# Performance work log

Hardware: AMD Instinct MI355X
Metric: run time of the kernel (lower is better)

## Reference

```python
import jax, jax.numpy as jnp
import numpy as np


def setup_inputs() -> dict:
    key = jax.random.key(0)
    k1, k2, k3, k4, k5, k6 = jax.random.split(key, 6)
    b, L, h, eh, M, N = 16, 256, 256, 64, 128, 128
    X = jax.random.normal(k1, (b, L, h), dtype=jnp.float32)
    E = jax.random.normal(k2, (b, L, L, eh), dtype=jnp.float32)
    A = jax.random.uniform(k3, (b, L, L), dtype=jnp.float32)
    w = jax.random.normal(k4, (b, L, 1), dtype=jnp.float32)
    mask = jnp.ones((b, L, L), dtype=bool)
    mol_lens = jax.random.randint(k5, (b, 2), 64, M + 1, dtype=jnp.int32)
    # force one row to the max so M,N match torch.max(mol_lens) exactly
    mol_lens = mol_lens.at[0].set(jnp.array([M, N], dtype=jnp.int32))
    return {"X": X, "E": E, "A": A, "w": w, "mask": mask,
            "mol_lens": mol_lens, "M": M, "N": N}


def reference(X, E, A, w, mask, mol_lens, M, N):
    b, L, h = X.shape
    eh = E.shape[-1]
    l0 = mol_lens[:, 0][:, None]            # [b,1]
    l1 = mol_lens[:, 1][:, None]
    p1 = jnp.arange(2 * M)[None, :]         # [1,2M]
    p2 = jnp.arange(2 * N)[None, :]         # [1,2N]

    # duplicate-and-pad source indices (note: X2 copies X[:, :l1], per source)
    src1 = jnp.clip(jnp.where(p1 < l0, p1, p1 - l0), 0, L - 1)          # [b,2M]
    srcX2 = jnp.clip(jnp.where(p2 < l1, p2, p2 - l1), 0, L - 1)         # [b,2N]
    srcE2 = jnp.clip(l0 + jnp.where(p2 < l1, p2, p2 - l1), 0, L - 1)    # [b,2N]
    valid1 = p1 < 2 * l0                    # [b,2M]
    valid2 = p2 < 2 * l1                    # [b,2N]

    bi = jnp.arange(b)[:, None]
    X1 = jnp.where(valid1[..., None], X[bi, src1], 0.0)                 # [b,2M,h]
    X2 = jnp.where(valid2[..., None], X[bi, srcX2], 0.0)                # [b,2N,h]

    # block-diagonal validity: (first copy x first copy) | (second x second)
    f1 = p1 < l0
    s1 = (p1 >= l0) & valid1
    blk1 = (f1[:, :, None] & f1[:, None, :]) | (s1[:, :, None] & s1[:, None, :])
    f2 = p2 < l1
    s2 = (p2 >= l1) & valid2
    blk2 = (f2[:, :, None] & f2[:, None, :]) | (s2[:, :, None] & s2[:, None, :])

    bii = jnp.arange(b)[:, None, None]
    g1 = E[bii, src1[:, :, None], src1[:, None, :]]                     # [b,2M,2M,eh]
    E1 = jnp.where(blk1[..., None], g1, 0.0)
    A1 = jnp.where(blk1, A[bii, src1[:, :, None], src1[:, None, :]], 0.0)
    g2 = E[bii, srcE2[:, :, None], srcE2[:, None, :]]                   # [b,2N,2N,eh]
    E2 = jnp.where(blk2[..., None], g2, 0.0)
    A2 = jnp.where(blk2, A[bii, srcE2[:, :, None], srcE2[:, None, :]], 0.0)

    w1 = jnp.zeros((b, 2 * M, 1), X.dtype)
    w2 = jnp.zeros((b, 2 * N, 1), X.dtype)

    # cross-copy masks on padded tensors
    mask1 = ~((f1[:, :, None] & s1[:, None, :]) | (s1[:, :, None] & f1[:, None, :]))
    mask2 = ~((f2[:, :, None] & s2[:, None, :]) | (s2[:, :, None] & f2[:, None, :]))

    # in-place edits of input mask: True on [:l0,:l0] and [l0:,l0:], False on cross
    q = jnp.arange(L)[None, :]
    lsum = l0 + l1
    left = q < l0                           # [b,L]
    midd = (q >= l0) & (q < lsum)
    cond_true = (left[:, :, None] & left[:, None, :]) | ((~left)[:, :, None] & (~left)[:, None, :])
    cond_false = (left[:, :, None] & midd[:, None, :]) | (midd[:, :, None] & left[:, None, :])
    mask_out = jnp.where(cond_true, True, jnp.where(cond_false, False, mask))

    return (X1, X2, E1, E2, A1, A2, mask1, mask2, w1, w2, mask_out)
```

## Files before the change

kernel.cpp:

```cpp
#include <hip/hip_runtime.h>


#define OFF_X1   0
#define OFF_X2   1048576
#define OFF_E1   2097152
#define OFF_E2   69206016
#define OFF_A1   136314880
#define OFF_A2   137363456
#define OFF_M1   138412032
#define OFF_M2   139460608
#define OFF_W1   140509184
#define OFF_MO   140517376

#define OFF_E1_V4 (OFF_E1 / 4)
#define OFF_E2_V4 (OFF_E2 / 4)

typedef float f32x4 __attribute__((ext_vector_type(4)));

__global__ __launch_bounds__(256) void fused_kernel(
    const f32x4* __restrict__ E,
    const float* __restrict__ X,
    const float* __restrict__ A,
    const int*   __restrict__ mask,
    const int*   __restrict__ mol_lens,
    float*       __restrict__ out)
{
    const int bb  = blockIdx.x;
    const int tid = threadIdx.x;

    const int i = bb >> 12;
    const int p = (bb >> 4) & 255;
    const int q = ((bb & 15) << 4) | (tid >> 4);
    const int c = tid & 15;
    const int t = bb * 256 + tid;

    const int l0 = mol_lens[i * 2];
    const int l1 = mol_lens[i * 2 + 1];

    f32x4* outv4 = (f32x4*)out;

    {
        const bool fp = p < l0, sp = !fp && (p < 2 * l0);
        const bool fq = q < l0, sq = !fq && (q < 2 * l0);
        f32x4 v = (f32x4)(0.f, 0.f, 0.f, 0.f);
        if ((fp && fq) || (sp && sq)) {
            const int ip = fp ? p : p - l0;
            const int iq = fq ? q : q - l0;
            v = E[((i * 256 + ip) * 256 + iq) * 16 + c];
        }
        __builtin_nontemporal_store(v, &outv4[OFF_E1_V4 + t]);
    }

    {
        const bool fp = p < l1, sp = !fp && (p < 2 * l1);
        const bool fq = q < l1, sq = !fq && (q < 2 * l1);
        f32x4 v = (f32x4)(0.f, 0.f, 0.f, 0.f);
        if ((fp && fq) || (sp && sq)) {
            int ip = l0 + (fp ? p : p - l1); if (ip > 255) ip = 255;
            int iq = l0 + (fq ? q : q - l1); if (iq > 255) iq = 255;
            v = E[((i * 256 + ip) * 256 + iq) * 16 + c];
        }
        __builtin_nontemporal_store(v, &outv4[OFF_E2_V4 + t]);
    }

    if (bb < 4096) {
        const int ts = t;
        const int qs = tid;
        const int ps = bb & 255;
        const int is = bb >> 8;

        const int sl0 = mol_lens[is * 2];
        const int sl1 = mol_lens[is * 2 + 1];

        const bool v1  = ps < 2 * sl0;
        const int  s1p = (ps < sl0) ? ps : ps - sl0;
        __builtin_nontemporal_store(
            v1 ? X[(is * 256 + s1p) * 256 + qs] : 0.f, &out[OFF_X1 + ts]);

        const bool v2  = ps < 2 * sl1;
        const int  s2p = (ps < sl1) ? ps : ps - sl1;
        __builtin_nontemporal_store(
            v2 ? X[(is * 256 + s2p) * 256 + qs] : 0.f, &out[OFF_X2 + ts]);

        const bool f1p = ps < sl0, s1pb = (!f1p) && v1;
        const bool f1q = qs < sl0, s1qb = (!f1q) && (qs < 2 * sl0);
        const int  s1q = f1q ? qs : qs - sl0;
        const bool blk1 = (f1p && f1q) || (s1pb && s1qb);
        __builtin_nontemporal_store(
            blk1 ? A[(is * 256 + s1p) * 256 + s1q] : 0.f, &out[OFF_A1 + ts]);
        __builtin_nontemporal_store(
            ((f1p && s1qb) || (s1pb && f1q)) ? 0.f : 1.f, &out[OFF_M1 + ts]);

        const bool f2p = ps < sl1, s2pb = (!f2p) && v2;
        const bool f2q = qs < sl1, s2qb = (!f2q) && (qs < 2 * sl1);
        int e2p = sl0 + (f2p ? ps : ps - sl1); if (e2p > 255) e2p = 255;
        int e2q = sl0 + (f2q ? qs : qs - sl1); if (e2q > 255) e2q = 255;
        const bool blk2 = (f2p && f2q) || (s2pb && s2qb);
        __builtin_nontemporal_store(
            blk2 ? A[(is * 256 + e2p) * 256 + e2q] : 0.f, &out[OFF_A2 + ts]);
        __builtin_nontemporal_store(
            ((f2p && s2qb) || (s2pb && f2q)) ? 0.f : 1.f, &out[OFF_M2 + ts]);

        const bool leftp = ps < sl0, leftq = qs < sl0;
        const int  lsum  = sl0 + sl1;
        const bool middp = (!leftp) && (ps < lsum);
        const bool middq = (!leftq) && (qs < lsum);
        const bool ct = (leftp && leftq) || ((!leftp) && (!leftq));
        const bool cf = (leftp && middq) || (middp && leftq);
        float mv;
        if (ct)      mv = 1.f;
        else if (cf) mv = 0.f;
        else         mv = (mask[ts] != 0) ? 1.f : 0.f;
        __builtin_nontemporal_store(mv, &out[OFF_MO + ts]);

        if (ts < 8192)
            __builtin_nontemporal_store(0.f, &out[OFF_W1 + ts]);
    }
}

extern "C" void kernel_launch(void* const* d_in, const int* in_sizes, int n_in,
                              void* d_out, int out_size, void* d_ws, size_t ws_size,
                              hipStream_t stream) {
    const float* X        = (const float*)d_in[0];
    const float* E        = (const float*)d_in[1];
    const float* A        = (const float*)d_in[2];
    const int*   mask     = (const int*)d_in[4];
    const int*   mol_lens = (const int*)d_in[5];

    float* out = (float*)d_out;

    fused_kernel<<<65536, 256, 0, stream>>>(
        (const f32x4*)E, X, A, mask, mol_lens, out);
}
```

Baseline: 694.5 us.

## Split E gather into separate kernel reading each source once, writing two copies

```diff
diff --git a/kernel.cpp b/kernel.cpp
--- a/kernel.cpp
+++ b/kernel.cpp
@@ -17,8 +17,7 @@
 
 typedef float f32x4 __attribute__((ext_vector_type(4)));
 
-__global__ __launch_bounds__(256) void fused_kernel(
-    const f32x4* __restrict__ E,
+__global__ __launch_bounds__(256) void fill_small_kernel(
     const float* __restrict__ X,
     const float* __restrict__ A,
     const int*   __restrict__ mask,
@@ -31,36 +30,25 @@
     const int i = bb >> 12;
     const int p = (bb >> 4) & 255;
     const int q = ((bb & 15) << 4) | (tid >> 4);
-    const int c = tid & 15;
     const int t = bb * 256 + tid;
 
     const int l0 = mol_lens[i * 2];
     const int l1 = mol_lens[i * 2 + 1];
 
     f32x4* outv4 = (f32x4*)out;
+    const f32x4 zero = (f32x4)(0.f, 0.f, 0.f, 0.f);
 
     {
         const bool fp = p < l0, sp = !fp && (p < 2 * l0);
         const bool fq = q < l0, sq = !fq && (q < 2 * l0);
-        f32x4 v = (f32x4)(0.f, 0.f, 0.f, 0.f);
-        if ((fp && fq) || (sp && sq)) {
-            const int ip = fp ? p : p - l0;
-            const int iq = fq ? q : q - l0;
-            v = E[((i * 256 + ip) * 256 + iq) * 16 + c];
-        }
-        __builtin_nontemporal_store(v, &outv4[OFF_E1_V4 + t]);
+        if (!((fp && fq) || (sp && sq)))
+            __builtin_nontemporal_store(zero, &outv4[OFF_E1_V4 + t]);
     }
-
     {
         const bool fp = p < l1, sp = !fp && (p < 2 * l1);
         const bool fq = q < l1, sq = !fq && (q < 2 * l1);
-        f32x4 v = (f32x4)(0.f, 0.f, 0.f, 0.f);
-        if ((fp && fq) || (sp && sq)) {
-            int ip = l0 + (fp ? p : p - l1); if (ip > 255) ip = 255;
-            int iq = l0 + (fq ? q : q - l1); if (iq > 255) iq = 255;
-            v = E[((i * 256 + ip) * 256 + iq) * 16 + c];
-        }
-        __builtin_nontemporal_store(v, &outv4[OFF_E2_V4 + t]);
+        if (!((fp && fq) || (sp && sq)))
+            __builtin_nontemporal_store(zero, &outv4[OFF_E2_V4 + t]);
     }
 
     if (bb < 4096) {
@@ -118,6 +106,47 @@
     }
 }
 
+__global__ __launch_bounds__(256) void gather_kernel(
+    const f32x4* __restrict__ E,
+    const int*   __restrict__ mol_lens,
+    float*       __restrict__ out)
+{
+    const int bb  = blockIdx.x;
+    const int tid = threadIdx.x;
+
+    const int c     = tid & 15;
+    const int iqo   = tid >> 4;
+    const int chunk = bb & 7;
+    const int ip    = (bb >> 3) & 127;
+    const int i     = bb >> 10;
+    const int iq    = chunk * 16 + iqo;
+
+    const int l0 = mol_lens[i * 2];
+    const int l1 = mol_lens[i * 2 + 1];
+
+    f32x4* outv4 = (f32x4*)out;
+
+    if (ip < l0) {
+        if (iq < l0) {
+            const f32x4 v = E[((i * 256 + ip) * 256 + iq) * 16 + c];
+            const int d1 = OFF_E1_V4 + ((i * 256 + ip) * 256 + iq) * 16 + c;
+            __builtin_nontemporal_store(v, &outv4[d1]);
+            const int d2 = OFF_E1_V4 + ((i * 256 + ip + l0) * 256 + (iq + l0)) * 16 + c;
+            __builtin_nontemporal_store(v, &outv4[d2]);
+        }
+    }
+
+    if (ip < l1) {
+        if (iq < l1) {
+            const f32x4 v = E[((i * 256 + l0 + ip) * 256 + (l0 + iq)) * 16 + c];
+            const int d1 = OFF_E2_V4 + ((i * 256 + ip) * 256 + iq) * 16 + c;
+            __builtin_nontemporal_store(v, &outv4[d1]);
+            const int d2 = OFF_E2_V4 + ((i * 256 + ip + l1) * 256 + (iq + l1)) * 16 + c;
+            __builtin_nontemporal_store(v, &outv4[d2]);
+        }
+    }
+}
+
 extern "C" void kernel_launch(void* const* d_in, const int* in_sizes, int n_in,
                               void* d_out, int out_size, void* d_ws, size_t ws_size,
                               hipStream_t stream) {
@@ -129,6 +158,7 @@
 
     float* out = (float*)d_out;
 
-    fused_kernel<<<65536, 256, 0, stream>>>(
-        (const f32x4*)E, X, A, mask, mol_lens, out);
+    fill_small_kernel<<<65536, 256, 0, stream>>>(X, A, mask, mol_lens, out);
+    gather_kernel<<<16384, 256, 0, stream>>>(
+        (const f32x4*)E, mol_lens, out);
 }
```

Result: no change. 705.3 us (+1.6%).

## Assign one E output row per block with precomputed source range

Applied to the files above, without the earlier changes.

```diff
diff --git a/kernel.cpp b/kernel.cpp
--- a/kernel.cpp
+++ b/kernel.cpp
@@ -17,7 +17,7 @@
 
 typedef float f32x4 __attribute__((ext_vector_type(4)));
 
-__global__ __launch_bounds__(256) void fused_kernel(
+__global__ __launch_bounds__(256) void fused_row_kernel(
     const f32x4* __restrict__ E,
     const float* __restrict__ X,
     const float* __restrict__ A,
@@ -28,46 +28,44 @@
     const int bb  = blockIdx.x;
     const int tid = threadIdx.x;
 
-    const int i = bb >> 12;
-    const int p = (bb >> 4) & 255;
-    const int q = ((bb & 15) << 4) | (tid >> 4);
-    const int c = tid & 15;
-    const int t = bb * 256 + tid;
+    f32x4* outv4 = (f32x4*)out;
+    const f32x4 zero = (f32x4)(0.f, 0.f, 0.f, 0.f);
 
-    const int l0 = mol_lens[i * 2];
-    const int l1 = mol_lens[i * 2 + 1];
+    if (bb < 8192) {
+        const int which = bb >> 12;
+        const int i     = (bb >> 8) & 15;
+        const int p     = bb & 255;
 
-    f32x4* outv4 = (f32x4*)out;
+        const int l0 = mol_lens[i * 2];
+        const int l1 = mol_lens[i * 2 + 1];
 
-    {
-        const bool fp = p < l0, sp = !fp && (p < 2 * l0);
-        const bool fq = q < l0, sq = !fq && (q < 2 * l0);
-        f32x4 v = (f32x4)(0.f, 0.f, 0.f, 0.f);
-        if ((fp && fq) || (sp && sq)) {
-            const int ip = fp ? p : p - l0;
-            const int iq = fq ? q : q - l0;
-            v = E[((i * 256 + ip) * 256 + iq) * 16 + c];
+        int q0 = 1, q1 = 0, srow = 0, sq0 = 0;
+        if (!which) {
+            if (p < l0)          { q0 = 0;  q1 = l0;     srow = p;            sq0 = 0; }
+            else if (p < 2 * l0) { q0 = l0; q1 = 2 * l0; srow = p - l0;       sq0 = 0; }
+        } else {
+            if (p < l1)          { q0 = 0;  q1 = l1;     srow = l0 + p;       sq0 = l0; }
+            else if (p < 2 * l1) { q0 = l1; q1 = 2 * l1; srow = l0 + p - l1;  sq0 = l0; }
         }
-        __builtin_nontemporal_store(v, &outv4[OFF_E1_V4 + t]);
-    }
 
-    {
-        const bool fp = p < l1, sp = !fp && (p < 2 * l1);
-        const bool fq = q < l1, sq = !fq && (q < 2 * l1);
-        f32x4 v = (f32x4)(0.f, 0.f, 0.f, 0.f);
-        if ((fp && fq) || (sp && sq)) {
-            int ip = l0 + (fp ? p : p - l1); if (ip > 255) ip = 255;
-            int iq = l0 + (fq ? q : q - l1); if (iq > 255) iq = 255;
-            v = E[((i * 256 + ip) * 256 + iq) * 16 + c];
+        const int out_base = (which ? OFF_E2_V4 : OFF_E1_V4) + (bb & 4095) * 4096;
+        const int src_base = ((i * 256 + srow) * 256 + sq0 - q0) * 16;
+
+        #pragma unroll
+        for (int it = 0; it < 16; ++it) {
+            const int f4 = it * 256 + tid;
+            const int q  = f4 >> 4;
+            f32x4 v = zero;
+            if (q >= q0 && q < q1)
+                v = E[src_base + f4];
+            __builtin_nontemporal_store(v, &outv4[out_base + f4]);
         }
-        __builtin_nontemporal_store(v, &outv4[OFF_E2_V4 + t]);
-    }
-
-    if (bb < 4096) {
-        const int ts = t;
-        const int qs = tid;
-        const int ps = bb & 255;
-        const int is = bb >> 8;
+    } else {
+        const int s   = bb - 8192;
+        const int qs  = tid;
+        const int ps  = s & 255;
+        const int is  = s >> 8;
+        const int ts  = s * 256 + tid;
 
         const int sl0 = mol_lens[is * 2];
         const int sl1 = mol_lens[is * 2 + 1];
@@ -129,6 +127,6 @@
 
     float* out = (float*)d_out;
 
-    fused_kernel<<<65536, 256, 0, stream>>>(
+    fused_row_kernel<<<12288, 256, 0, stream>>>(
         (const f32x4*)E, X, A, mask, mol_lens, out);
 }
```

Result: no change. 708.3 us (+2.0%).
